# Performance work log

Measured on AMD Instinct MI355X. Metric: run time of the kernel, lower is better.

The kernel has to match this reference:

```python
import jax, jax.numpy as jnp
import numpy as np


def setup_inputs() -> dict:
    key = jax.random.key(0)
    k1, k2 = jax.random.split(key)
    h = jax.random.normal(k1, (8, 16, 64, 512), dtype=jnp.float32)
    M = jax.random.normal(k2, (20000, 512), dtype=jnp.float32)
    return {"h": h, "M": M}


def reference(h, M):
    # h: [B, T, X, R], M: [K, R]
    B, T, X, R = h.shape
    hf = h.reshape(-1, R)                      # [N, R]
    att = jax.nn.softmax(hf @ M.T, axis=1)     # [N, K], unscaled dot-product
    out = att @ M                              # [N, R]
    return out.reshape(B, T, X, R)
```

## Files before the change

kernel.cpp:

```cpp
#include <hip/hip_runtime.h>
#include <stdint.h>

#define NQ 8192
#define NK 20000
#define RD 512
#define NT 157

typedef float f32x4 __attribute__((ext_vector_type(4)));
typedef short s16x8 __attribute__((ext_vector_type(8)));

__device__ __forceinline__ unsigned short bf16_rn(float x) {
    uint32_t u = __float_as_uint(x);
    return (unsigned short)((u + 0x7FFFu + ((u >> 16) & 1)) >> 16);
}

__global__ void preconv_kernel(const float* __restrict__ M,
                               unsigned short* __restrict__ Mhi,
                               unsigned short* __restrict__ Mlo,
                               unsigned short* __restrict__ MT) {
    __shared__ float tilef[64 * 65];
    const int k0 = blockIdx.x * 64, r0 = blockIdx.y * 64;
    const int t = threadIdx.x;
#pragma unroll
    for (int i = 0; i < 16; i++) {
        int e = t + i * 256;
        int kr = e >> 6, cc = e & 63;
        int key = k0 + kr;
        if (key < NK) {
            float x = M[(size_t)key * RD + r0 + cc];
            uint32_t u = __float_as_uint(x);
            Mhi[(size_t)key * RD + r0 + cc] = (unsigned short)(u >> 16);
            Mlo[(size_t)key * RD + r0 + cc] = bf16_rn(x - __uint_as_float(u & 0xFFFF0000u));
            tilef[cc * 65 + kr] = x;
        }
    }
    __syncthreads();
#pragma unroll
    for (int i = 0; i < 16; i++) {
        int e = t + i * 256;
        int rr = e >> 6, kk = e & 63;
        int key = k0 + kk;
        if (key < NK) MT[(size_t)(r0 + rr) * NK + key] = bf16_rn(tilef[rr * 65 + kk]);
    }
}

__global__ __launch_bounds__(512, 2) void flash3_kernel(
        const float* __restrict__ h,
        const unsigned short* __restrict__ Mhi,
        const unsigned short* __restrict__ Mlo,
        const unsigned short* __restrict__ MT,
        float* __restrict__ out) {
    __shared__ unsigned short qbuf[2 * 16 * 512 * 2];
    __shared__ unsigned short pbuf[8 * 64 * 8];
    __shared__ float smaxb[8 * 2 * 16];
    __shared__ float ssumb[8 * 2 * 16];

    const int tid = threadIdx.x;
    const int ch = tid >> 6, l = tid & 63;
    const int l15 = l & 15, q4 = l >> 4;
    const int qbase = blockIdx.x * 32;

#pragma unroll
    for (int i = 0; i < 4; i++) {
        int g = tid + i * 512;
        int row = g >> 6, s = (g >> 2) & 15, qg = g & 3;
        int strip = row >> 4, lrow = row & 15;
        const float* src = h + (size_t)(qbase + row) * RD + s * 32 + qg * 8;
        f32x4 a = *(const f32x4*)src;
        f32x4 b = *(const f32x4*)(src + 4);
        s16x8 hi8, lo8;
#pragma unroll
        for (int j = 0; j < 8; j++) {
            float x = (j < 4) ? a[j] : b[j - 4];
            uint32_t u = __float_as_uint(x);
            hi8[j] = (short)(u >> 16);
            lo8[j] = (short)bf16_rn(x - __uint_as_float(u & 0xFFFF0000u));
        }
        int off = ((strip * 16 + s) * 512 + (qg * 16 + lrow) * 8);
        *(s16x8*)&qbuf[off] = hi8;
        *(s16x8*)&qbuf[16384 + off] = lo8;
    }
    __syncthreads();

    f32x4 O[2][4];
#pragma unroll
    for (int st = 0; st < 2; st++)
#pragma unroll
        for (int ct = 0; ct < 4; ct++) O[st][ct] = 0.f;
    f32x4 m_run[2], l_run[2];
    m_run[0] = -3e38f; m_run[1] = -3e38f; l_run[0] = 0.f; l_run[1] = 0.f;

    s16x8 khq[2], klq[2];
    {
        const size_t b0 = (size_t)(ch * 16 + l15) * RD + q4 * 8;
        khq[0] = *(const s16x8*)(Mhi + b0);
        klq[0] = *(const s16x8*)(Mlo + b0);
        khq[1] = *(const s16x8*)(Mhi + b0 + 32);
        klq[1] = *(const s16x8*)(Mlo + b0 + 32);
    }

    for (int tile = 0; tile < NT; tile++) {
        const int keyg = tile * 128 + ch * 16 + l15;
        const unsigned short* kph = Mhi + (size_t)keyg * RD + q4 * 8;
        const unsigned short* kpl = Mlo + (size_t)keyg * RD + q4 * 8;

        f32x4 Ca = 0.f, Cb = 0.f;
#pragma unroll
        for (int s = 0; s < 16; s++) {
            s16x8 kh = khq[s & 1], kl = klq[s & 1];
            if (s < 14) {
                khq[s & 1] = *(const s16x8*)(kph + (s + 2) * 32);
                klq[s & 1] = *(const s16x8*)(kpl + (s + 2) * 32);
            }
            s16x8 qh0 = *(const s16x8*)&qbuf[s * 512 + l * 8];
            s16x8 ql0 = *(const s16x8*)&qbuf[16384 + s * 512 + l * 8];
            s16x8 qh1 = *(const s16x8*)&qbuf[(16 + s) * 512 + l * 8];
            s16x8 ql1 = *(const s16x8*)&qbuf[16384 + (16 + s) * 512 + l * 8];
            Ca = __builtin_amdgcn_mfma_f32_16x16x32_bf16(qh0, kh, Ca, 0, 0, 0);
            Cb = __builtin_amdgcn_mfma_f32_16x16x32_bf16(qh1, kh, Cb, 0, 0, 0);
            Ca = __builtin_amdgcn_mfma_f32_16x16x32_bf16(ql0, kh, Ca, 0, 0, 0);
            Cb = __builtin_amdgcn_mfma_f32_16x16x32_bf16(ql1, kh, Cb, 0, 0, 0);
            Ca = __builtin_amdgcn_mfma_f32_16x16x32_bf16(qh0, kl, Ca, 0, 0, 0);
            Cb = __builtin_amdgcn_mfma_f32_16x16x32_bf16(qh1, kl, Cb, 0, 0, 0);
        }
        if (tile == NT - 1) {
            if (keyg >= NK) { Ca = -3e38f; Cb = -3e38f; }
        }

        const unsigned short* mtp = MT + (size_t)(ch * 64 + l15) * NK + tile * 128 + q4 * 8;
        s16x8 btC[4];
#pragma unroll
        for (int sk = 0; sk < 4; sk++) btC[sk] = *(const s16x8*)(mtp + sk * 32);

        f32x4 mx[2]; mx[0] = Ca; mx[1] = Cb;
#pragma unroll
        for (int d = 1; d < 16; d <<= 1) {
#pragma unroll
            for (int v = 0; v < 4; v++) {
                mx[0][v] = fmaxf(mx[0][v], __shfl_xor(mx[0][v], d, 16));
                mx[1][v] = fmaxf(mx[1][v], __shfl_xor(mx[1][v], d, 16));
            }
        }
        if (l15 == 0) {
            *(f32x4*)&smaxb[(ch * 2 + 0) * 16 + q4 * 4] = mx[0];
            *(f32x4*)&smaxb[(ch * 2 + 1) * 16 + q4 * 4] = mx[1];
        }
        __syncthreads();
        f32x4 mnew[2]; mnew[0] = m_run[0]; mnew[1] = m_run[1];
#pragma unroll
        for (int cc = 0; cc < 8; cc++) {
#pragma unroll
            for (int st = 0; st < 2; st++) {
                f32x4 tv = *(const f32x4*)&smaxb[(cc * 2 + st) * 16 + q4 * 4];
#pragma unroll
                for (int v = 0; v < 4; v++) mnew[st][v] = fmaxf(mnew[st][v], tv[v]);
            }
        }
        f32x4 alpha[2];
#pragma unroll
        for (int st = 0; st < 2; st++)
#pragma unroll
            for (int v = 0; v < 4; v++) {
                alpha[st][v] = __expf(m_run[st][v] - mnew[st][v]);
                m_run[st][v] = mnew[st][v];
            }
        const int key_loc = ch * 16 + l15;
        const int sk0 = key_loc >> 5, kq = (key_loc >> 3) & 3, jj = key_loc & 7;
        f32x4 ps[2]; ps[0] = 0.f; ps[1] = 0.f;
#pragma unroll
        for (int st = 0; st < 2; st++) {
#pragma unroll
            for (int v = 0; v < 4; v++) {
                float sv = (st == 0) ? Ca[v] : Cb[v];
                float p = __expf(sv - mnew[st][v]);
                ps[st][v] += p;
                pbuf[((sk0 * 2 + st) * 64 + (q4 * 4 + v) + 16 * kq) * 8 + jj] = bf16_rn(p);
            }
        }
#pragma unroll
        for (int d = 1; d < 16; d <<= 1) {
#pragma unroll
            for (int v = 0; v < 4; v++) {
                ps[0][v] += __shfl_xor(ps[0][v], d, 16);
                ps[1][v] += __shfl_xor(ps[1][v], d, 16);
            }
        }
        if (l15 == 0) {
            *(f32x4*)&ssumb[(ch * 2 + 0) * 16 + q4 * 4] = ps[0];
            *(f32x4*)&ssumb[(ch * 2 + 1) * 16 + q4 * 4] = ps[1];
        }
        __syncthreads();
        f32x4 ts[2]; ts[0] = 0.f; ts[1] = 0.f;
#pragma unroll
        for (int cc = 0; cc < 8; cc++) {
            ts[0] += *(const f32x4*)&ssumb[(cc * 2 + 0) * 16 + q4 * 4];
            ts[1] += *(const f32x4*)&ssumb[(cc * 2 + 1) * 16 + q4 * 4];
        }
#pragma unroll
        for (int st = 0; st < 2; st++)
#pragma unroll
            for (int v = 0; v < 4; v++) l_run[st][v] = l_run[st][v] * alpha[st][v] + ts[st][v];
#pragma unroll
        for (int st = 0; st < 2; st++)
#pragma unroll
            for (int ct = 0; ct < 4; ct++)
#pragma unroll
                for (int v = 0; v < 4; v++) O[st][ct][v] *= alpha[st][v];
        s16x8 pa[2][4];
#pragma unroll
        for (int st = 0; st < 2; st++)
#pragma unroll
            for (int sk = 0; sk < 4; sk++)
                pa[st][sk] = *(const s16x8*)&pbuf[((sk * 2 + st) * 64 + l) * 8];

        if (tile < NT - 1) {
            const size_t b2 = (size_t)(tile * 128 + 128 + ch * 16 + l15) * RD + q4 * 8;
            khq[0] = *(const s16x8*)(Mhi + b2);
            klq[0] = *(const s16x8*)(Mlo + b2);
            khq[1] = *(const s16x8*)(Mhi + b2 + 32);
            klq[1] = *(const s16x8*)(Mlo + b2 + 32);
        }

#pragma unroll
        for (int ct = 0; ct < 4; ct++) {
            s16x8 btN[4];
            if (ct < 3) {
#pragma unroll
                for (int sk = 0; sk < 4; sk++)
                    btN[sk] = *(const s16x8*)(mtp + (size_t)(ct + 1) * 16 * NK + sk * 32);
            }
#pragma unroll
            for (int sk = 0; sk < 4; sk++) {
                O[0][ct] = __builtin_amdgcn_mfma_f32_16x16x32_bf16(pa[0][sk], btC[sk], O[0][ct], 0, 0, 0);
                O[1][ct] = __builtin_amdgcn_mfma_f32_16x16x32_bf16(pa[1][sk], btC[sk], O[1][ct], 0, 0, 0);
            }
            if (ct < 3) {
#pragma unroll
                for (int sk = 0; sk < 4; sk++) btC[sk] = btN[sk];
            }
        }
    }

#pragma unroll
    for (int st = 0; st < 2; st++)
#pragma unroll
        for (int ct = 0; ct < 4; ct++)
#pragma unroll
            for (int v = 0; v < 4; v++)
                out[(size_t)(qbase + st * 16 + q4 * 4 + v) * RD + (ch * 4 + ct) * 16 + l15] =
                    O[st][ct][v] / l_run[st][v];
}

__global__ __launch_bounds__(256) void naive_kernel(const float* __restrict__ h,
                                                    const float* __restrict__ M,
                                                    float* __restrict__ out) {
    __shared__ float hs[16 * 520];
    __shared__ float ms[8 * 520];
    __shared__ float sdot[2][128];
    __shared__ float sm[16], sl[16], sal[16], sp[16][8];
    const int t = threadIdx.x;
    const int qbase = blockIdx.x * 16;
#pragma unroll
    for (int i = 0; i < 32; i++) {
        int e = t + i * 256;
        int row = e >> 9, col = e & 511;
        hs[row * 520 + col] = h[(size_t)(qbase + row) * RD + col];
    }
    if (t < 16) { sm[t] = -3e38f; sl[t] = 0.f; }
    float Oacc[32];
#pragma unroll
    for (int i = 0; i < 32; i++) Oacc[i] = 0.f;
    const int q = t >> 4;
    const int eb = (t & 15) * 32;

    for (int k0 = 0; k0 < NK; k0 += 8) {
        __syncthreads();
#pragma unroll
        for (int i = 0; i < 16; i++) {
            int e = t + i * 256;
            if (e < 4096) {
                int kk = e >> 9, col = e & 511;
                ms[kk * 520 + col] = M[(size_t)(k0 + kk) * RD + col];
            }
        }
        __syncthreads();
        {
            int pair = t & 127, half = t >> 7;
            int qq = pair & 15, kk = pair >> 4;
            const float* hp = &hs[qq * 520 + half * 256];
            const float* mp = &ms[kk * 520 + half * 256];
            float acc = 0.f;
#pragma unroll 8
            for (int e = 0; e < 256; e++) acc += hp[e] * mp[e];
            sdot[half][pair] = acc;
        }
        __syncthreads();
        if (t < 16) {
            int qq = t;
            float s8[8];
#pragma unroll
            for (int kk = 0; kk < 8; kk++) s8[kk] = sdot[0][qq + 16 * kk] + sdot[1][qq + 16 * kk];
            float mn = sm[qq];
#pragma unroll
            for (int kk = 0; kk < 8; kk++) mn = fmaxf(mn, s8[kk]);
            float al = __expf(sm[qq] - mn);
            float addl = 0.f;
#pragma unroll
            for (int kk = 0; kk < 8; kk++) { float p = __expf(s8[kk] - mn); sp[qq][kk] = p; addl += p; }
            sm[qq] = mn; sl[qq] = sl[qq] * al + addl; sal[qq] = al;
        }
        __syncthreads();
        {
            float al = sal[q];
#pragma unroll
            for (int i = 0; i < 32; i++) Oacc[i] *= al;
#pragma unroll
            for (int kk = 0; kk < 8; kk++) {
                float p = sp[q][kk];
                const float* mp = &ms[kk * 520 + eb];
#pragma unroll
                for (int i = 0; i < 32; i++) Oacc[i] += p * mp[i];
            }
        }
    }
    __syncthreads();
    float inv = 1.f / sl[q];
#pragma unroll
    for (int i = 0; i < 32; i++) out[(size_t)(qbase + q) * RD + eb + i] = Oacc[i] * inv;
}

extern "C" void kernel_launch(void* const* d_in, const int* in_sizes, int n_in,
                              void* d_out, int out_size, void* d_ws, size_t ws_size,
                              hipStream_t stream) {
    const float* h = (const float*)d_in[0];
    const float* M = (const float*)d_in[1];
    float* out = (float*)d_out;
    const size_t seg = (size_t)NK * RD;
    const size_t need = (seg * 3ull + 8192ull) * 2ull;

    if (ws_size >= need) {
        unsigned short* Mhi = (unsigned short*)d_ws;
        unsigned short* Mlo = Mhi + seg;
        unsigned short* MT  = Mlo + seg;
        preconv_kernel<<<dim3(313, 8), 256, 0, stream>>>(M, Mhi, Mlo, MT);
        flash3_kernel<<<256, 512, 0, stream>>>(h, Mhi, Mlo, MT, out);
    } else {
        naive_kernel<<<512, 256, 0, stream>>>(h, M, out);
    }
}
```

Measured before the change: 1.858 ms.

## Stream K and MT tiles into an LDS ring with async global-to-LDS loads

The flash-attention kernel now processes 256 keys per tile instead of 128, which halves the number of outer iterations and block-wide softmax barriers. Key (hi/lo) and transposed-value fragments are no longer loaded into registers. They are streamed into a per-wave double-buffered LDS ring using global_load_lds, with hand-placed s_waitcnt so the next fragments load while MFMAs run. The QK and PV phases chain their prefetches so the next tile's keys are issued during the current PV pass. The cost is more LDS, which rules out two blocks per CU, plus fragile manual wait counts and padded tail reads that rely on masking.

Result: faster. 1.782 ms (-4.1%).

```diff
diff --git a/kernel.cpp b/kernel.cpp
--- a/kernel.cpp
+++ b/kernel.cpp
@@ -4,7 +4,8 @@
 #define NQ 8192
 #define NK 20000
 #define RD 512
-#define NT 157
+#define KN 256
+#define NTT 79
 
 typedef float f32x4 __attribute__((ext_vector_type(4)));
 typedef short s16x8 __attribute__((ext_vector_type(8)));
@@ -12,6 +13,22 @@
 __device__ __forceinline__ unsigned short bf16_rn(float x) {
     uint32_t u = __float_as_uint(x);
     return (unsigned short)((u + 0x7FFFu + ((u >> 16) & 1)) >> 16);
+}
+
+__device__ __forceinline__ void lds_barrier() {
+    asm volatile("s_waitcnt lgkmcnt(0)\n\ts_barrier" ::: "memory");
+}
+__device__ __forceinline__ void wait_vm4() {
+    asm volatile("s_waitcnt vmcnt(4)" ::: "memory");
+}
+__device__ __forceinline__ void wait_lgkm0() {
+    asm volatile("s_waitcnt lgkmcnt(0)" ::: "memory");
+}
+
+__device__ __forceinline__ void gload_lds16(const unsigned short* g, unsigned short* lds) {
+    __builtin_amdgcn_global_load_lds(
+        (const __attribute__((address_space(1))) uint32_t*)g,
+        (__attribute__((address_space(3))) uint32_t*)lds, 16, 0, 0);
 }
 
 __global__ void preconv_kernel(const float* __restrict__ M,
@@ -44,20 +61,22 @@
     }
 }
 
-__global__ __launch_bounds__(512, 2) void flash3_kernel(
+__global__ __launch_bounds__(512, 2) void flash8_kernel(
         const float* __restrict__ h,
         const unsigned short* __restrict__ Mhi,
         const unsigned short* __restrict__ Mlo,
         const unsigned short* __restrict__ MT,
         float* __restrict__ out) {
-    __shared__ unsigned short qbuf[2 * 16 * 512 * 2];
-    __shared__ unsigned short pbuf[8 * 64 * 8];
+    __shared__ unsigned short qbuf[32768];
+    __shared__ unsigned short kring[8][8][512];
+    __shared__ unsigned short pbuf[16 * 512];
     __shared__ float smaxb[8 * 2 * 16];
     __shared__ float ssumb[8 * 2 * 16];
 
     const int tid = threadIdx.x;
-    const int ch = tid >> 6, l = tid & 63;
+    const int w = tid >> 6, l = tid & 63;
     const int l15 = l & 15, q4 = l >> 4;
+    const int kq = (l15 >> 3) & 1, jj = l15 & 7;
     const int qbase = blockIdx.x * 32;
 
 #pragma unroll
@@ -80,7 +99,28 @@
         *(s16x8*)&qbuf[off] = hi8;
         *(s16x8*)&qbuf[16384 + off] = lo8;
     }
-    __syncthreads();
+
+    const unsigned short* mtw = MT + (size_t)(w * 64 + l15) * NK + q4 * 8;
+    auto issueK = [&](int t2, int s2) {
+        if (t2 >= NTT) t2 = NTT - 1;
+        int b = (s2 & 1) * 4;
+        const size_t off = (size_t)(t2 * KN + w * 32 + l15) * RD + s2 * 32 + q4 * 8;
+        gload_lds16(Mhi + off, &kring[w][b + 0][0]);
+        gload_lds16(Mhi + off + (size_t)16 * RD, &kring[w][b + 1][0]);
+        gload_lds16(Mlo + off, &kring[w][b + 2][0]);
+        gload_lds16(Mlo + off + (size_t)16 * RD, &kring[w][b + 3][0]);
+    };
+    auto issuePV = [&](int t2, int sk2) {
+        int b = (sk2 & 1) * 4;
+        const unsigned short* g = mtw + (size_t)t2 * KN + sk2 * 32;
+#pragma unroll
+        for (int ct = 0; ct < 4; ct++)
+            gload_lds16(g + (size_t)ct * 16 * NK, &kring[w][b + ct][0]);
+    };
+
+    issueK(0, 0);
+    issueK(0, 1);
+    lds_barrier();
 
     f32x4 O[2][4];
 #pragma unroll
@@ -90,62 +130,62 @@
     f32x4 m_run[2], l_run[2];
     m_run[0] = -3e38f; m_run[1] = -3e38f; l_run[0] = 0.f; l_run[1] = 0.f;
 
-    s16x8 khq[2], klq[2];
-    {
-        const size_t b0 = (size_t)(ch * 16 + l15) * RD + q4 * 8;
-        khq[0] = *(const s16x8*)(Mhi + b0);
-        klq[0] = *(const s16x8*)(Mlo + b0);
-        khq[1] = *(const s16x8*)(Mhi + b0 + 32);
-        klq[1] = *(const s16x8*)(Mlo + b0 + 32);
-    }
-
-    for (int tile = 0; tile < NT; tile++) {
-        const int keyg = tile * 128 + ch * 16 + l15;
-        const unsigned short* kph = Mhi + (size_t)keyg * RD + q4 * 8;
-        const unsigned short* kpl = Mlo + (size_t)keyg * RD + q4 * 8;
-
-        f32x4 Ca = 0.f, Cb = 0.f;
+    for (int tile = 0; tile < NTT; tile++) {
+        f32x4 C[2][2];
+        C[0][0] = 0.f; C[0][1] = 0.f; C[1][0] = 0.f; C[1][1] = 0.f;
 #pragma unroll
         for (int s = 0; s < 16; s++) {
-            s16x8 kh = khq[s & 1], kl = klq[s & 1];
-            if (s < 14) {
-                khq[s & 1] = *(const s16x8*)(kph + (s + 2) * 32);
-                klq[s & 1] = *(const s16x8*)(kpl + (s + 2) * 32);
-            }
+            wait_vm4();
+            const int b = (s & 1) * 4;
+            s16x8 kh0 = *(const s16x8*)&kring[w][b + 0][l * 8];
+            s16x8 kh1 = *(const s16x8*)&kring[w][b + 1][l * 8];
+            s16x8 kl0 = *(const s16x8*)&kring[w][b + 2][l * 8];
+            s16x8 kl1 = *(const s16x8*)&kring[w][b + 3][l * 8];
             s16x8 qh0 = *(const s16x8*)&qbuf[s * 512 + l * 8];
             s16x8 ql0 = *(const s16x8*)&qbuf[16384 + s * 512 + l * 8];
             s16x8 qh1 = *(const s16x8*)&qbuf[(16 + s) * 512 + l * 8];
             s16x8 ql1 = *(const s16x8*)&qbuf[16384 + (16 + s) * 512 + l * 8];
-            Ca = __builtin_amdgcn_mfma_f32_16x16x32_bf16(qh0, kh, Ca, 0, 0, 0);
-            Cb = __builtin_amdgcn_mfma_f32_16x16x32_bf16(qh1, kh, Cb, 0, 0, 0);
-            Ca = __builtin_amdgcn_mfma_f32_16x16x32_bf16(ql0, kh, Ca, 0, 0, 0);
-            Cb = __builtin_amdgcn_mfma_f32_16x16x32_bf16(ql1, kh, Cb, 0, 0, 0);
-            Ca = __builtin_amdgcn_mfma_f32_16x16x32_bf16(qh0, kl, Ca, 0, 0, 0);
-            Cb = __builtin_amdgcn_mfma_f32_16x16x32_bf16(qh1, kl, Cb, 0, 0, 0);
-        }
-        if (tile == NT - 1) {
-            if (keyg >= NK) { Ca = -3e38f; Cb = -3e38f; }
-        }
-
-        const unsigned short* mtp = MT + (size_t)(ch * 64 + l15) * NK + tile * 128 + q4 * 8;
-        s16x8 btC[4];
-#pragma unroll
-        for (int sk = 0; sk < 4; sk++) btC[sk] = *(const s16x8*)(mtp + sk * 32);
-
-        f32x4 mx[2]; mx[0] = Ca; mx[1] = Cb;
+            wait_lgkm0();
+            if (s < 14) issueK(tile, s + 2);
+            else issuePV(tile, s - 14);
+            C[0][0] = __builtin_amdgcn_mfma_f32_16x16x32_bf16(qh0, kh0, C[0][0], 0, 0, 0);
+            C[1][0] = __builtin_amdgcn_mfma_f32_16x16x32_bf16(qh1, kh0, C[1][0], 0, 0, 0);
+            C[0][1] = __builtin_amdgcn_mfma_f32_16x16x32_bf16(qh0, kh1, C[0][1], 0, 0, 0);
+            C[1][1] = __builtin_amdgcn_mfma_f32_16x16x32_bf16(qh1, kh1, C[1][1], 0, 0, 0);
+            C[0][0] = __builtin_amdgcn_mfma_f32_16x16x32_bf16(ql0, kh0, C[0][0], 0, 0, 0);
+            C[1][0] = __builtin_amdgcn_mfma_f32_16x16x32_bf16(ql1, kh0, C[1][0], 0, 0, 0);
+            C[0][1] = __builtin_amdgcn_mfma_f32_16x16x32_bf16(ql0, kh1, C[0][1], 0, 0, 0);
+            C[1][1] = __builtin_amdgcn_mfma_f32_16x16x32_bf16(ql1, kh1, C[1][1], 0, 0, 0);
+            C[0][0] = __builtin_amdgcn_mfma_f32_16x16x32_bf16(qh0, kl0, C[0][0], 0, 0, 0);
+            C[1][0] = __builtin_amdgcn_mfma_f32_16x16x32_bf16(qh1, kl0, C[1][0], 0, 0, 0);
+            C[0][1] = __builtin_amdgcn_mfma_f32_16x16x32_bf16(qh0, kl1, C[0][1], 0, 0, 0);
+            C[1][1] = __builtin_amdgcn_mfma_f32_16x16x32_bf16(qh1, kl1, C[1][1], 0, 0, 0);
+        }
+        if (tile == NTT - 1) {
+#pragma unroll
+            for (int cb = 0; cb < 2; cb++) {
+                int kg = tile * KN + w * 32 + cb * 16 + l15;
+                if (kg >= NK) { C[0][cb] = -3e38f; C[1][cb] = -3e38f; }
+            }
+        }
+
+        f32x4 mx[2];
+#pragma unroll
+        for (int st = 0; st < 2; st++)
+#pragma unroll
+            for (int v = 0; v < 4; v++) mx[st][v] = fmaxf(C[st][0][v], C[st][1][v]);
 #pragma unroll
         for (int d = 1; d < 16; d <<= 1) {
 #pragma unroll
-            for (int v = 0; v < 4; v++) {
-                mx[0][v] = fmaxf(mx[0][v], __shfl_xor(mx[0][v], d, 16));
-                mx[1][v] = fmaxf(mx[1][v], __shfl_xor(mx[1][v], d, 16));
-            }
+            for (int st = 0; st < 2; st++)
+#pragma unroll
+                for (int v = 0; v < 4; v++) mx[st][v] = fmaxf(mx[st][v], __shfl_xor(mx[st][v], d, 16));
         }
         if (l15 == 0) {
-            *(f32x4*)&smaxb[(ch * 2 + 0) * 16 + q4 * 4] = mx[0];
-            *(f32x4*)&smaxb[(ch * 2 + 1) * 16 + q4 * 4] = mx[1];
-        }
-        __syncthreads();
+            *(f32x4*)&smaxb[(w * 2 + 0) * 16 + q4 * 4] = mx[0];
+            *(f32x4*)&smaxb[(w * 2 + 1) * 16 + q4 * 4] = mx[1];
+        }
+        lds_barrier();
         f32x4 mnew[2]; mnew[0] = m_run[0]; mnew[1] = m_run[1];
 #pragma unroll
         for (int cc = 0; cc < 8; cc++) {
@@ -164,32 +204,31 @@
                 alpha[st][v] = __expf(m_run[st][v] - mnew[st][v]);
                 m_run[st][v] = mnew[st][v];
             }
-        const int key_loc = ch * 16 + l15;
-        const int sk0 = key_loc >> 5, kq = (key_loc >> 3) & 3, jj = key_loc & 7;
         f32x4 ps[2]; ps[0] = 0.f; ps[1] = 0.f;
 #pragma unroll
         for (int st = 0; st < 2; st++) {
 #pragma unroll
-            for (int v = 0; v < 4; v++) {
-                float sv = (st == 0) ? Ca[v] : Cb[v];
-                float p = __expf(sv - mnew[st][v]);
-                ps[st][v] += p;
-                pbuf[((sk0 * 2 + st) * 64 + (q4 * 4 + v) + 16 * kq) * 8 + jj] = bf16_rn(p);
+            for (int cb = 0; cb < 2; cb++) {
+#pragma unroll
+                for (int v = 0; v < 4; v++) {
+                    float p = __expf(C[st][cb][v] - mnew[st][v]);
+                    ps[st][v] += p;
+                    pbuf[(w * 2 + st) * 512 + ((cb * 2 + kq) * 16 + q4 * 4 + v) * 8 + jj] = bf16_rn(p);
+                }
             }
         }
 #pragma unroll
         for (int d = 1; d < 16; d <<= 1) {
 #pragma unroll
-            for (int v = 0; v < 4; v++) {
-                ps[0][v] += __shfl_xor(ps[0][v], d, 16);
-                ps[1][v] += __shfl_xor(ps[1][v], d, 16);
-            }
+            for (int st = 0; st < 2; st++)
+#pragma unroll
+                for (int v = 0; v < 4; v++) ps[st][v] += __shfl_xor(ps[st][v], d, 16);
         }
         if (l15 == 0) {
-            *(f32x4*)&ssumb[(ch * 2 + 0) * 16 + q4 * 4] = ps[0];
-            *(f32x4*)&ssumb[(ch * 2 + 1) * 16 + q4 * 4] = ps[1];
-        }
-        __syncthreads();
+            *(f32x4*)&ssumb[(w * 2 + 0) * 16 + q4 * 4] = ps[0];
+            *(f32x4*)&ssumb[(w * 2 + 1) * 16 + q4 * 4] = ps[1];
+        }
+        lds_barrier();
         f32x4 ts[2]; ts[0] = 0.f; ts[1] = 0.f;
 #pragma unroll
         for (int cc = 0; cc < 8; cc++) {
@@ -206,39 +245,30 @@
             for (int ct = 0; ct < 4; ct++)
 #pragma unroll
                 for (int v = 0; v < 4; v++) O[st][ct][v] *= alpha[st][v];
-        s16x8 pa[2][4];
-#pragma unroll
-        for (int st = 0; st < 2; st++)
-#pragma unroll
-            for (int sk = 0; sk < 4; sk++)
-                pa[st][sk] = *(const s16x8*)&pbuf[((sk * 2 + st) * 64 + l) * 8];
-
-        if (tile < NT - 1) {
-            const size_t b2 = (size_t)(tile * 128 + 128 + ch * 16 + l15) * RD + q4 * 8;
-            khq[0] = *(const s16x8*)(Mhi + b2);
-            klq[0] = *(const s16x8*)(Mlo + b2);
-            khq[1] = *(const s16x8*)(Mhi + b2 + 32);
-            klq[1] = *(const s16x8*)(Mlo + b2 + 32);
-        }
-
-#pragma unroll
-        for (int ct = 0; ct < 4; ct++) {
-            s16x8 btN[4];
-            if (ct < 3) {
-#pragma unroll
-                for (int sk = 0; sk < 4; sk++)
-                    btN[sk] = *(const s16x8*)(mtp + (size_t)(ct + 1) * 16 * NK + sk * 32);
-            }
-#pragma unroll
-            for (int sk = 0; sk < 4; sk++) {
-                O[0][ct] = __builtin_amdgcn_mfma_f32_16x16x32_bf16(pa[0][sk], btC[sk], O[0][ct], 0, 0, 0);
-                O[1][ct] = __builtin_amdgcn_mfma_f32_16x16x32_bf16(pa[1][sk], btC[sk], O[1][ct], 0, 0, 0);
-            }
-            if (ct < 3) {
-#pragma unroll
-                for (int sk = 0; sk < 4; sk++) btC[sk] = btN[sk];
-            }
-        }
+
+#pragma unroll
+        for (int sk = 0; sk < 8; sk++) {
+            wait_vm4();
+            const int b = (sk & 1) * 4;
+            s16x8 bt0 = *(const s16x8*)&kring[w][b + 0][l * 8];
+            s16x8 bt1 = *(const s16x8*)&kring[w][b + 1][l * 8];
+            s16x8 bt2 = *(const s16x8*)&kring[w][b + 2][l * 8];
+            s16x8 bt3 = *(const s16x8*)&kring[w][b + 3][l * 8];
+            s16x8 pa0 = *(const s16x8*)&pbuf[(sk * 2 + 0) * 512 + l * 8];
+            s16x8 pa1 = *(const s16x8*)&pbuf[(sk * 2 + 1) * 512 + l * 8];
+            wait_lgkm0();
+            if (sk < 6) issuePV(tile, sk + 2);
+            else issueK(tile + 1, sk - 6);
+            O[0][0] = __builtin_amdgcn_mfma_f32_16x16x32_bf16(pa0, bt0, O[0][0], 0, 0, 0);
+            O[1][0] = __builtin_amdgcn_mfma_f32_16x16x32_bf16(pa1, bt0, O[1][0], 0, 0, 0);
+            O[0][1] = __builtin_amdgcn_mfma_f32_16x16x32_bf16(pa0, bt1, O[0][1], 0, 0, 0);
+            O[1][1] = __builtin_amdgcn_mfma_f32_16x16x32_bf16(pa1, bt1, O[1][1], 0, 0, 0);
+            O[0][2] = __builtin_amdgcn_mfma_f32_16x16x32_bf16(pa0, bt2, O[0][2], 0, 0, 0);
+            O[1][2] = __builtin_amdgcn_mfma_f32_16x16x32_bf16(pa1, bt2, O[1][2], 0, 0, 0);
+            O[0][3] = __builtin_amdgcn_mfma_f32_16x16x32_bf16(pa0, bt3, O[0][3], 0, 0, 0);
+            O[1][3] = __builtin_amdgcn_mfma_f32_16x16x32_bf16(pa1, bt3, O[1][3], 0, 0, 0);
+        }
+        lds_barrier();
     }
 
 #pragma unroll
@@ -247,7 +277,7 @@
         for (int ct = 0; ct < 4; ct++)
 #pragma unroll
             for (int v = 0; v < 4; v++)
-                out[(size_t)(qbase + st * 16 + q4 * 4 + v) * RD + (ch * 4 + ct) * 16 + l15] =
+                out[(size_t)(qbase + st * 16 + q4 * 4 + v) * RD + w * 64 + ct * 16 + l15] =
                     O[st][ct][v] / l_run[st][v];
 }
 
@@ -343,7 +373,7 @@
         unsigned short* Mlo = Mhi + seg;
         unsigned short* MT  = Mlo + seg;
         preconv_kernel<<<dim3(313, 8), 256, 0, stream>>>(M, Mhi, Mlo, MT);
-        flash3_kernel<<<256, 512, 0, stream>>>(h, Mhi, Mlo, MT, out);
+        flash8_kernel<<<256, 512, 0, stream>>>(h, Mhi, Mlo, MT, out);
     } else {
         naive_kernel<<<512, 256, 0, stream>>>(h, M, out);
     }
```
